# Optimization experiments

Measured on AMD Instinct MI355X. Metric: run time of the kernel, lower is better.

Reference implementation:

```python
import jax, jax.numpy as jnp
import numpy as np

H, HEADS, LAYERS = 512, 4, 3
HD = H // HEADS
FFN = 4 * H
B, S = 4, 2048
EPS = 1e-5
SCALE_BASE = 512.0
GAMMAS = (1.0 - np.exp(np.linspace(np.log(1.0 / 32.0), np.log(1.0 / 512.0), HEADS))).astype(np.float32)


def _xpos(x, downscale):
    # x: [B, heads, L, d]; standard XPOS rotary with per-dim decay scale
    L, d = x.shape[-2], x.shape[-1]
    half = d // 2
    s = (jnp.arange(half, dtype=jnp.float32) + 0.4 * d) / (1.4 * d)          # [half]
    pos = jnp.arange(L, dtype=jnp.float32)
    scale = s[None, :] ** (pos[:, None] / SCALE_BASE)                         # [L, half]
    inv_freq = 1.0 / (10000.0 ** (jnp.arange(half, dtype=jnp.float32) / half))
    ang = pos[:, None] * inv_freq[None, :]                                    # [L, half]
    if downscale:
        scale = 1.0 / scale
    sin_s = jnp.repeat(jnp.sin(ang) * scale, 2, axis=-1)                      # [L, d]
    cos_s = jnp.repeat(jnp.cos(ang) * scale, 2, axis=-1)
    x1, x2 = x[..., 0::2], x[..., 1::2]
    rot = jnp.stack([-x2, x1], axis=-1).reshape(x.shape)                      # rotate_every_two
    return x * cos_s + rot * sin_s


def _layernorm(x, w, b):
    m = x.mean(-1, keepdims=True)
    v = ((x - m) ** 2).mean(-1, keepdims=True)
    return (x - m) / jnp.sqrt(v + EPS) * w + b


def _decay_mask(L):
    n = jnp.arange(L)
    nm = n[:, None] - n[None, :]
    g = jnp.asarray(GAMMAS)                                                   # [heads]
    # D[h,n,m] = gamma_h^(n-m) for n>=m else 0
    return jnp.where((nm >= 0)[None], g[:, None, None] ** jnp.maximum(nm, 0)[None], 0.0)


def _msr(X, WQ, WK, WV, WG, WO, gnw, gnb, D):
    # X: [B,S,H]; WQ/WK/WV: [heads,H,HD]; D: [heads,S,S]
    Q = _xpos(jnp.einsum('bsh,nhd->bnsd', X, WQ), False)
    K = _xpos(jnp.einsum('bsh,nhd->bnsd', X, WK), True)
    V = jnp.einsum('bsh,nhd->bnsd', X, WV)
    A = jnp.einsum('bnsd,bntd->bnst', Q, K) * D[None]                          # decay-weighted retention
    Y = jnp.einsum('bnst,bntd->bnsd', A, V)                                    # [B,heads,S,HD]
    Y = jnp.transpose(Y, (0, 2, 1, 3))                                         # [B,S,heads,HD] (head-major concat)
    m = Y.mean(-1, keepdims=True)
    v = ((Y - m) ** 2).mean(-1, keepdims=True)
    Yn = ((Y - m) / jnp.sqrt(v + EPS)).reshape(X.shape[0], X.shape[1], H) * gnw + gnb  # GroupNorm(heads, H)
    G = X @ WG
    return (G * jax.nn.sigmoid(G) * Yn) @ WO                                   # swish gate + out proj


def setup_inputs() -> dict:
    key = jax.random.key(0)
    ks = jax.random.split(key, 10)
    rn = lambda k, shape, sc: jax.random.normal(k, shape, jnp.float32) * sc
    return {
        'X': rn(ks[0], (B, S, H), 1.0),
        'WQ': rn(ks[1], (LAYERS, HEADS, H, HD), 1.0 / H),
        'WK': rn(ks[2], (LAYERS, HEADS, H, HD), 1.0 / H),
        'WV': rn(ks[3], (LAYERS, HEADS, H, HD), 1.0 / H),
        'WG': rn(ks[4], (LAYERS, H, H), 1.0 / H),
        'WO': rn(ks[5], (LAYERS, H, H), 1.0 / H),
        'gn_w': jnp.ones((LAYERS, H), jnp.float32),
        'gn_b': jnp.zeros((LAYERS, H), jnp.float32),
        'ln1_w': jnp.ones((LAYERS, H), jnp.float32),
        'ln1_b': jnp.zeros((LAYERS, H), jnp.float32),
        'ln2_w': jnp.ones((LAYERS, H), jnp.float32),
        'ln2_b': jnp.zeros((LAYERS, H), jnp.float32),
        'ffn_w1': rn(ks[6], (LAYERS, H, FFN), (2.0 / (H + FFN)) ** 0.5),
        'ffn_b1': jnp.zeros((LAYERS, FFN), jnp.float32),
        'ffn_w2': rn(ks[7], (LAYERS, FFN, H), (2.0 / (H + FFN)) ** 0.5),
        'ffn_b2': jnp.zeros((LAYERS, H), jnp.float32),
    }


def reference(X, WQ, WK, WV, WG, WO, gn_w, gn_b, ln1_w, ln1_b, ln2_w, ln2_b, ffn_w1, ffn_b1, ffn_w2, ffn_b2):
    D = _decay_mask(X.shape[1])
    for l in range(LAYERS):
        Y = _msr(_layernorm(X, ln1_w[l], ln1_b[l]), WQ[l], WK[l], WV[l], WG[l], WO[l], gn_w[l], gn_b[l], D) + X
        Hn = _layernorm(Y, ln2_w[l], ln2_b[l])
        X = jax.nn.gelu(Hn @ ffn_w1[l] + ffn_b1[l], approximate=False) @ ffn_w2[l] + ffn_b2[l] + Y
    return X, jnp.einsum('bsh,bth->bst', X, X)
```

## Files before the change

### kernel.cpp

```cpp
#include <hip/hip_runtime.h>
#include <math.h>

#define HH 512
#define NHEADS 4
#define HD 128
#define HALF 64
#define FFND 2048
#define BB 4
#define SS 2048
#define NLAYERS 3
#define ROWS (BB*SS)
#define EPSF 1e-5f
#define QKVGW 2048

typedef float f32x4 __attribute__((ext_vector_type(4)));
typedef float f32x16 __attribute__((ext_vector_type(16)));
typedef __bf16 bf16x8 __attribute__((ext_vector_type(8)));
typedef unsigned u32x2 __attribute__((ext_vector_type(2)));

__device__ __forceinline__ unsigned short f2bf(float f) {
    union { float f; unsigned u; } v; v.f = f;
    unsigned r = (v.u + 0x7FFFu + ((v.u >> 16) & 1u)) >> 16;
    return (unsigned short)r;
}
__device__ __forceinline__ float bf2f(unsigned short h) {
    union { unsigned u; float f; } v; v.u = ((unsigned)h) << 16;
    return v.f;
}
__device__ __forceinline__ void gl16(const void* g, void* l) {
    __builtin_amdgcn_global_load_lds((const __attribute__((address_space(1))) void*)g,
                                     (__attribute__((address_space(3))) void*)l, 16, 0, 0);
}
__device__ __forceinline__ bf16x8 ld8(const void* p) { return *(const bf16x8*)p; }
__device__ __forceinline__ unsigned laddr(void* p) {
    return (unsigned)(size_t)(__attribute__((address_space(3))) char*)p;
}
__device__ __forceinline__ u32x2 tr8(unsigned a) {
    u32x2 r;
    asm volatile("ds_read_b64_tr_b16 %0, %1" : "=v"(r) : "v"(a));
    return r;
}

__global__ void k_tables(float* __restrict__ cq, float* __restrict__ sq,
                         float* __restrict__ ck, float* __restrict__ sk) {
    int i = threadIdx.x;
    int s = blockIdx.x;
    float si   = ((float)i + 0.4f * (float)HD) / (1.4f * (float)HD);
    float scale = powf(si, (float)s / 512.0f);
    float invf = powf(10000.0f, -((float)i) / (float)HALF);
    float ang  = (float)s * invf;
    float c = cosf(ang), sn = sinf(ang);
    int idx = s * HALF + i;
    cq[idx] = c * scale;   sq[idx] = sn * scale;
    float is = 1.0f / scale;
    ck[idx] = c * is;      sk[idx] = sn * is;
}

__global__ __launch_bounds__(256) void k_wt(const float* __restrict__ src, unsigned short* __restrict__ dst,
                                            int K, int N, int zn, size_t sL, size_t sZ) {
    __shared__ float T[32][33];
    int n0 = blockIdx.x * 32, k0 = blockIdx.y * 32;
    int z = blockIdx.z;
    src += (size_t)z * (size_t)K * N;
    dst += (size_t)(z / zn) * sL + (size_t)(z % zn) * sZ;
    int tx = threadIdx.x & 31, ty = threadIdx.x >> 5;
    #pragma unroll
    for (int i = 0; i < 4; ++i) {
        int r = ty + i * 8;
        T[r][tx] = src[(size_t)(k0 + r) * N + n0 + tx];
    }
    __syncthreads();
    #pragma unroll
    for (int i = 0; i < 4; ++i) {
        int r = ty + i * 8;
        dst[(size_t)(n0 + r) * K + k0 + tx] = f2bf(T[tx][r]);
    }
}

__global__ __launch_bounds__(256) void k_ln(const float* __restrict__ x, const float* __restrict__ w,
                                            const float* __restrict__ b, unsigned short* __restrict__ y) {
    int lane = threadIdx.x & 63;
    size_t row = (size_t)blockIdx.x * 4 + (threadIdx.x >> 6);
    const float4* xr = (const float4*)(x + row * HH);
    float4 v0 = xr[lane * 2];
    float4 v1 = xr[lane * 2 + 1];
    float s  = v0.x + v0.y + v0.z + v0.w + v1.x + v1.y + v1.z + v1.w;
    float ss = v0.x*v0.x + v0.y*v0.y + v0.z*v0.z + v0.w*v0.w
             + v1.x*v1.x + v1.y*v1.y + v1.z*v1.z + v1.w*v1.w;
    for (int off = 32; off > 0; off >>= 1) {
        s  += __shfl_xor(s, off);
        ss += __shfl_xor(ss, off);
    }
    float m   = s * (1.0f / HH);
    float var = ss * (1.0f / HH) - m * m;
    float inv = rsqrtf(var + EPSF);
    int h0 = lane * 8;
    float4 wa = *(const float4*)(w + h0);
    float4 wb = *(const float4*)(w + h0 + 4);
    float4 ba = *(const float4*)(b + h0);
    float4 bb2 = *(const float4*)(b + h0 + 4);
    uint4 pk;
    pk.x = f2bf((v0.x - m) * inv * wa.x + ba.x) | ((unsigned)f2bf((v0.y - m) * inv * wa.y + ba.y) << 16);
    pk.y = f2bf((v0.z - m) * inv * wa.z + ba.z) | ((unsigned)f2bf((v0.w - m) * inv * wa.w + ba.w) << 16);
    pk.z = f2bf((v1.x - m) * inv * wb.x + bb2.x) | ((unsigned)f2bf((v1.y - m) * inv * wb.y + bb2.y) << 16);
    pk.w = f2bf((v1.z - m) * inv * wb.z + bb2.z) | ((unsigned)f2bf((v1.w - m) * inv * wb.w + bb2.w) << 16);
    *(uint4*)(y + row * HH + h0) = pk;
}

__global__ __launch_bounds__(256) void k_xpos(unsigned short* __restrict__ QG,
    const float* __restrict__ cq, const float* __restrict__ sq,
    const float* __restrict__ ck, const float* __restrict__ sk) {
    int row = blockIdx.x, p = threadIdx.x;
    int s = row & (SS - 1), n = p >> 6, i = p & 63;
    int ti = s * HALF + i;
    size_t qo = (size_t)row * QKVGW + n * HD + i * 2;
    unsigned qv = *(unsigned*)(QG + qo);
    float x1 = bf2f(qv & 0xffff), x2 = bf2f(qv >> 16);
    float c = cq[ti], sn = sq[ti];
    *(unsigned*)(QG + qo) = (unsigned)f2bf(x1 * c - x2 * sn) | ((unsigned)f2bf(x2 * c + x1 * sn) << 16);
    size_t ko = qo + 512;
    unsigned kv = *(unsigned*)(QG + ko);
    x1 = bf2f(kv & 0xffff); x2 = bf2f(kv >> 16);
    c = ck[ti]; sn = sk[ti];
    *(unsigned*)(QG + ko) = (unsigned)f2bf(x1 * c - x2 * sn) | ((unsigned)f2bf(x2 * c + x1 * sn) << 16);
}

__global__ __launch_bounds__(128, 2) void k_ret(
    const unsigned short* __restrict__ QG, float* __restrict__ Y) {
    __shared__ __align__(16) char sm[40960];
    const int tid = threadIdx.x;
    const int lane = tid & 63, wv = tid >> 6;
    const int l31 = lane & 31, g2 = lane >> 5;
    const int b4 = (lane >> 4) & 1;
    const int xs = (int)gridDim.x - 1 - (int)blockIdx.x;
    const int hn = blockIdx.y, b = blockIdx.z;
    const int s0 = xs * 64;
    const double la = -3.4657359027997265, lb = -6.238324625039508;
    const float gamma = (float)(1.0 - exp(la + (lb - la) * ((double)hn / 3.0)));
    const float l2g = log2f(gamma);
    const size_t rowbase = (size_t)b * SS;
    const int qcol = hn * HD, kcol = 512 + hn * HD, vcol = 1024 + hn * HD;
    const char* Gp = (const char*)QG;

    const int srow = s0 + wv * 32 + l31;
    bf16x8 qf[8];
    #pragma unroll
    for (int kc = 0; kc < 8; ++kc)
        qf[kc] = ld8(QG + (rowbase + srow) * QKVGW + qcol + kc * 16 + g2 * 8);

    float gq[4], gj[4];
    #pragma unroll
    for (int q = 0; q < 4; ++q) { gq[q] = exp2f(-l2g * (8.0f * q)); gj[q] = exp2f(-l2g * (float)q); }
    const float gt32m = exp2f(-l2g * 32.0f);

    f32x16 accy[4];
    #pragma unroll
    for (int d = 0; d < 4; ++d)
        #pragma unroll
        for (int e = 0; e < 16; ++e) accy[d][e] = 0.0f;

    const int sloc = wv * 32 + l31;
    const int ssw = (sloc & 7) << 4;
    const int r15 = (l31 & 15) << 4;
    const unsigned vbase = laddr(sm + 16384) + b4 * 2048 + g2 * 256 + (lane & 15) * 2;
    const int nt = xs + 1;

    for (int t = 0; t < nt; ++t) {
        const int t0 = t * 64;
        __syncthreads();
        #pragma unroll
        for (int c = 0; c < 8; ++c) {
            int chunk = wv * 8 + c;
            int r = chunk * 4 + (lane >> 4);
            int w = ((lane & 15) * 16) ^ ((r & 15) << 4);
            gl16(Gp + ((rowbase + t0 + r) * QKVGW + kcol) * 2 + w, sm + chunk * 1024);
        }
        #pragma unroll
        for (int c = 0; c < 8; ++c) {
            int chunk = wv * 8 + c;
            int slot = chunk * 64 + lane;
            int sub = slot >> 3, w8 = slot & 7;
            int db = sub >> 4, tb = sub & 15;
            int tl = tb * 4 + (w8 >> 1);
            int d  = db * 16 + (w8 & 1) * 8;
            gl16(Gp + ((rowbase + t0 + tl) * QKVGW + vcol + d) * 2, sm + 16384 + chunk * 1024);
        }
        __syncthreads();
        f32x16 pacc0, pacc1;
        #pragma unroll
        for (int e = 0; e < 16; ++e) { pacc0[e] = 0.0f; pacc1[e] = 0.0f; }
        #pragma unroll
        for (int kc = 0; kc < 8; ++kc) {
            bf16x8 k0 = ld8(sm + l31 * 256 + ((kc * 32 + g2 * 16) ^ r15));
            bf16x8 k1 = ld8(sm + (32 + l31) * 256 + ((kc * 32 + g2 * 16) ^ r15));
            pacc0 = __builtin_amdgcn_mfma_f32_32x32x16_bf16(k0, qf[kc], pacc0, 0, 0, 0);
            pacc1 = __builtin_amdgcn_mfma_f32_32x32x16_bf16(k1, qf[kc], pacc1, 0, 0, 0);
        }
        const float G0 = exp2f(l2g * (float)(srow - t0 - g2 * 4));
        #pragma unroll
        for (int tb2 = 0; tb2 < 2; ++tb2) {
            const float gb = tb2 ? gt32m : 1.0f;
            #pragma unroll
            for (int q = 0; q < 4; ++q) {
                unsigned short u0, u1, u2, u3;
                int tbase = t0 + tb2 * 32 + q * 8 + g2 * 4;
                float base = G0 * gb * gq[q];
                float p0 = (tb2 ? pacc1 : pacc0)[q * 4 + 0];
                float p1 = (tb2 ? pacc1 : pacc0)[q * 4 + 1];
                float p2 = (tb2 ? pacc1 : pacc0)[q * 4 + 2];
                float p3 = (tb2 ? pacc1 : pacc0)[q * 4 + 3];
                u0 = f2bf((srow >= tbase + 0) ? p0 * base * gj[0] : 0.0f);
                u1 = f2bf((srow >= tbase + 1) ? p1 * base * gj[1] : 0.0f);
                u2 = f2bf((srow >= tbase + 2) ? p2 * base * gj[2] : 0.0f);
                u3 = f2bf((srow >= tbase + 3) ? p3 * base * gj[3] : 0.0f);
                u32x2 pk2;
                pk2.x = (unsigned)u0 | ((unsigned)u1 << 16);
                pk2.y = (unsigned)u2 | ((unsigned)u3 << 16);
                *(u32x2*)(sm + 32768 + ((sloc * 128 + tb2 * 64 + q * 16 + g2 * 8) ^ ssw)) = pk2;
            }
        }
        bf16x8 pf[4];
        #pragma unroll
        for (int tc = 0; tc < 4; ++tc)
            pf[tc] = ld8(sm + 32768 + ((sloc * 128 + tc * 32 + g2 * 16) ^ ssw));
        #pragma unroll
        for (int dblk = 0; dblk < 4; ++dblk) {
            u32x2 va[4], vb[4];
            #pragma unroll
            for (int tc = 0; tc < 4; ++tc) {
                unsigned a0 = vbase + dblk * 4096 + tc * 512;
                va[tc] = tr8(a0);
                vb[tc] = tr8(a0 + 128);
            }
            asm volatile("s_waitcnt lgkmcnt(0)" ::: "memory");
            __builtin_amdgcn_sched_barrier(0);
            #pragma unroll
            for (int tc = 0; tc < 4; ++tc) {
                union { u32x2 u[2]; bf16x8 v; } cvt;
                cvt.u[0] = va[tc]; cvt.u[1] = vb[tc];
                accy[dblk] = __builtin_amdgcn_mfma_f32_32x32x16_bf16(pf[tc], cvt.v, accy[dblk], 0, 0, 0);
            }
        }
    }
    #pragma unroll
    for (int dblk = 0; dblk < 4; ++dblk)
        #pragma unroll
        for (int rg = 0; rg < 16; ++rg) {
            int sl2 = s0 + wv * 32 + (rg & 3) + (rg >> 2) * 8 + g2 * 4;
            Y[(rowbase + sl2) * HH + hn * HD + dblk * 32 + l31] = accy[dblk][rg];
        }
}

__global__ __launch_bounds__(256) void k_gate(
    const float* __restrict__ Yr, const unsigned short* __restrict__ QG,
    const float* __restrict__ gw, const float* __restrict__ gb,
    unsigned short* __restrict__ E) {
    int lane = threadIdx.x & 63;
    int grp  = blockIdx.x * 4 + (threadIdx.x >> 6);
    int row = grp >> 2, nh = grp & 3;
    size_t off = (size_t)row * HH + nh * HD + lane * 2;
    float2 v = *(const float2*)(Yr + off);
    float s = v.x + v.y, ss = v.x * v.x + v.y * v.y;
    for (int o = 32; o > 0; o >>= 1) {
        s  += __shfl_xor(s, o);
        ss += __shfl_xor(ss, o);
    }
    float m   = s * (1.0f / HD);
    float var = ss * (1.0f / HD) - m * m;
    float inv = rsqrtf(var + EPSF);
    int h = nh * HD + lane * 2;
    unsigned gv = *(const unsigned*)(QG + (size_t)row * QKVGW + 1536 + nh * HD + lane * 2);
    float g0 = bf2f(gv & 0xffff), g1 = bf2f(gv >> 16);
    float2 w2 = *(const float2*)(gw + h), b2 = *(const float2*)(gb + h);
    float yn0 = (v.x - m) * inv * w2.x + b2.x;
    float yn1 = (v.y - m) * inv * w2.y + b2.y;
    float e0v = g0 / (1.0f + expf(-g0)) * yn0;
    float e1v = g1 / (1.0f + expf(-g1)) * yn1;
    *(unsigned*)(E + off) = (unsigned)f2bf(e0v) | ((unsigned)f2bf(e1v) << 16);
}

__global__ __launch_bounds__(256) void k_cast(const float* __restrict__ x, unsigned short* __restrict__ y) {
    size_t i = ((size_t)blockIdx.x * 256 + threadIdx.x) * 8;
    float4 a = *(const float4*)(x + i), c = *(const float4*)(x + i + 4);
    uint4 pk;
    pk.x = f2bf(a.x) | ((unsigned)f2bf(a.y) << 16);
    pk.y = f2bf(a.z) | ((unsigned)f2bf(a.w) << 16);
    pk.z = f2bf(c.x) | ((unsigned)f2bf(c.y) << 16);
    pk.w = f2bf(c.z) | ((unsigned)f2bf(c.w) << 16);
    *(uint4*)(y + i) = pk;
}

template<int EPI, int OUTBF>
__global__ __launch_bounds__(256) void k_mm(
    const unsigned short* __restrict__ A, const unsigned short* __restrict__ Bt,
    void* __restrict__ Cv, const float* __restrict__ bias, const float* __restrict__ Rs,
    int M, int N, int K, size_t aB, size_t bB, size_t cB) {
    __shared__ __align__(16) char sm[16384];
    const int tid = threadIdx.x;
    const int lane = tid & 63, wid = tid >> 6;
    const int wr = wid >> 1, wc = wid & 1;
    const int lcol = lane & 15, lrow = lane >> 4;
    const size_t m0 = (size_t)blockIdx.x * 128, n0 = (size_t)blockIdx.y * 128;
    const char* Ab = (const char*)(A + (size_t)blockIdx.z * aB);
    const char* Bb = (const char*)(Bt + (size_t)blockIdx.z * bB);
    f32x4 acc[4][4];
    #pragma unroll
    for (int i = 0; i < 4; ++i)
        #pragma unroll
        for (int j = 0; j < 4; ++j) acc[i][j] = f32x4{0.f, 0.f, 0.f, 0.f};
    for (int k0 = 0; k0 < K; k0 += 32) {
        __syncthreads();
        #pragma unroll
        for (int c = 0; c < 2; ++c) {
            int chunk = wid * 2 + c;
            int r = chunk * 16 + (lane >> 2);
            int w = ((lane & 3) ^ (r & 3)) << 4;
            gl16(Ab + ((size_t)(m0 + r) * K + k0) * 2 + w, sm + chunk * 1024);
            gl16(Bb + ((size_t)(n0 + r) * K + k0) * 2 + w, sm + 8192 + chunk * 1024);
        }
        __syncthreads();
        bf16x8 af[4], bfr[4];
        #pragma unroll
        for (int m = 0; m < 4; ++m) {
            int r = wr * 64 + m * 16 + lcol;
            af[m] = ld8(sm + r * 64 + ((lrow * 16) ^ ((r & 3) << 4)));
        }
        #pragma unroll
        for (int n2 = 0; n2 < 4; ++n2) {
            int r = wc * 64 + n2 * 16 + lcol;
            bfr[n2] = ld8(sm + 8192 + r * 64 + ((lrow * 16) ^ ((r & 3) << 4)));
        }
        #pragma unroll
        for (int m = 0; m < 4; ++m)
            #pragma unroll
            for (int n2 = 0; n2 < 4; ++n2)
                acc[m][n2] = __builtin_amdgcn_mfma_f32_16x16x32_bf16(af[m], bfr[n2], acc[m][n2], 0, 0, 0);
    }
    float* Cf = (float*)Cv + (size_t)blockIdx.z * cB;
    unsigned short* Cb = (unsigned short*)Cv + (size_t)blockIdx.z * cB;
    const float* Rb = (EPI >= 2) ? (Rs + (size_t)blockIdx.z * cB) : nullptr;
    #pragma unroll
    for (int m = 0; m < 4; ++m) {
        #pragma unroll
        for (int n2 = 0; n2 < 4; ++n2) {
            size_t col = n0 + wc * 64 + n2 * 16 + lcol;
            float bc = (EPI == 1 || EPI == 2) ? bias[col] : 0.0f;
            #pragma unroll
            for (int j = 0; j < 4; ++j) {
                size_t row = m0 + wr * 64 + m * 16 + lrow * 4 + j;
                float v = acc[m][n2][j];
                if (EPI == 1) { v += bc; v = 0.5f * v * (1.0f + erff(v * 0.70710678118654752f)); }
                else if (EPI == 2) v += bc + Rb[row * N + col];
                else if (EPI == 3) v += Rb[row * N + col];
                if (OUTBF) Cb[row * N + col] = f2bf(v);
                else       Cf[row * N + col] = v;
            }
        }
    }
}

extern "C" void kernel_launch(void* const* d_in, const int* in_sizes, int n_in,
                              void* d_out, int out_size, void* d_ws, size_t ws_size,
                              hipStream_t stream) {
    const float* X0  = (const float*)d_in[0];
    const float* WQ  = (const float*)d_in[1];
    const float* WK  = (const float*)d_in[2];
    const float* WV  = (const float*)d_in[3];
    const float* WG  = (const float*)d_in[4];
    const float* WO  = (const float*)d_in[5];
    const float* gnw = (const float*)d_in[6];
    const float* gnb = (const float*)d_in[7];
    const float* l1w = (const float*)d_in[8];
    const float* l1b = (const float*)d_in[9];
    const float* l2w = (const float*)d_in[10];
    const float* l2b = (const float*)d_in[11];
    const float* fw1 = (const float*)d_in[12];
    const float* fb1 = (const float*)d_in[13];
    const float* fw2 = (const float*)d_in[14];
    const float* fb2 = (const float*)d_in[15];
    float* outX = (float*)d_out;
    float* outG = outX + (size_t)ROWS * HH;

    char* wp = (char*)d_ws;
    auto take = [&](size_t bytes) { char* p = wp; wp += (bytes + 255) & ~(size_t)255; return p; };
    float* cq = (float*)take((size_t)SS * HALF * 4);
    float* sq = (float*)take((size_t)SS * HALF * 4);
    float* ck = (float*)take((size_t)SS * HALF * 4);
    float* sk = (float*)take((size_t)SS * HALF * 4);
    unsigned short* Wcat = (unsigned short*)take((size_t)NLAYERS * QKVGW * HH * 2);
    unsigned short* WOt = (unsigned short*)take((size_t)NLAYERS * HH * HH * 2);
    unsigned short* F1t = (unsigned short*)take((size_t)NLAYERS * HH * FFND * 2);
    unsigned short* F2t = (unsigned short*)take((size_t)NLAYERS * HH * FFND * 2);
    unsigned short* Xn  = (unsigned short*)take((size_t)ROWS * HH * 2);
    unsigned short* QKVG = (unsigned short*)take((size_t)ROWS * QKVGW * 2);
    unsigned short* Eb  = (unsigned short*)take((size_t)ROWS * HH * 2);
    float* Yr   = (float*)take((size_t)ROWS * HH * 4);
    float* Y2   = (float*)take((size_t)ROWS * HH * 4);
    float* Xbuf = (float*)take((size_t)ROWS * HH * 4);
    unsigned short* Hb = (unsigned short*)take((size_t)ROWS * FFND * 2);
    unsigned short* Xb = Xn;

    k_tables<<<SS, HALF, 0, stream>>>(cq, sq, ck, sk);
    k_wt<<<dim3(4, 16, 12), 256, 0, stream>>>(WQ, Wcat, HH, HD, 4, (size_t)QKVGW * HH, (size_t)HD * HH);
    k_wt<<<dim3(4, 16, 12), 256, 0, stream>>>(WK, Wcat + (size_t)512 * HH, HH, HD, 4, (size_t)QKVGW * HH, (size_t)HD * HH);
    k_wt<<<dim3(4, 16, 12), 256, 0, stream>>>(WV, Wcat + (size_t)1024 * HH, HH, HD, 4, (size_t)QKVGW * HH, (size_t)HD * HH);
    k_wt<<<dim3(16, 16, 3), 256, 0, stream>>>(WG, Wcat + (size_t)1536 * HH, HH, HH, 1, (size_t)QKVGW * HH, 0);
    k_wt<<<dim3(16, 16, 3), 256, 0, stream>>>(WO, WOt, HH, HH, 1, (size_t)HH * HH, 0);
    k_wt<<<dim3(64, 16, 3), 256, 0, stream>>>(fw1, F1t, HH, FFND, 1, (size_t)HH * FFND, 0);
    k_wt<<<dim3(16, 64, 3), 256, 0, stream>>>(fw2, F2t, FFND, HH, 1, (size_t)FFND * HH, 0);

    const float* curX = X0;
    for (int l = 0; l < NLAYERS; ++l) {
        const unsigned short* Bc = Wcat + (size_t)l * QKVGW * HH;
        const unsigned short* Bo = WOt + (size_t)l * HH * HH;
        const unsigned short* B1 = F1t + (size_t)l * HH * FFND;
        const unsigned short* B2 = F2t + (size_t)l * HH * FFND;
        k_ln<<<ROWS / 4, 256, 0, stream>>>(curX, l1w + l * HH, l1b + l * HH, Xn);
        dim3 gq(ROWS / 128, QKVGW / 128, 1);
        k_mm<0, 1><<<gq, 256, 0, stream>>>(Xn, Bc, QKVG, nullptr, nullptr, ROWS, QKVGW, HH, 0, 0, 0);
        k_xpos<<<ROWS, 256, 0, stream>>>(QKVG, cq, sq, ck, sk);
        k_ret<<<dim3(SS / 64, NHEADS, BB), 128, 0, stream>>>(QKVG, Yr);
        k_gate<<<ROWS, 256, 0, stream>>>(Yr, QKVG, gnw + l * HH, gnb + l * HH, Eb);
        dim3 g1(ROWS / 128, HH / 128, 1);
        k_mm<3, 0><<<g1, 256, 0, stream>>>(Eb, Bo, Y2, nullptr, curX, ROWS, HH, HH, 0, 0, 0);
        k_ln<<<ROWS / 4, 256, 0, stream>>>(Y2, l2w + l * HH, l2b + l * HH, Xn);
        dim3 g2(ROWS / 128, FFND / 128, 1);
        k_mm<1, 1><<<g2, 256, 0, stream>>>(Xn, B1, Hb, fb1 + (size_t)l * FFND, nullptr, ROWS, FFND, HH, 0, 0, 0);
        float* newX = (l == NLAYERS - 1) ? outX : Xbuf;
        k_mm<2, 0><<<g1, 256, 0, stream>>>(Hb, B2, newX, fb2 + (size_t)l * HH, Y2, ROWS, HH, FFND, 0, 0, 0);
        curX = newX;
    }
    k_cast<<<ROWS * HH / (256 * 8), 256, 0, stream>>>(outX, Xb);
    dim3 g3(SS / 128, SS / 128, BB);
    k_mm<0, 0><<<g3, 256, 0, stream>>>(Xb, Xb, outG, nullptr, nullptr, SS, SS, HH,
                                       (size_t)SS * HH, (size_t)SS * HH, (size_t)SS * SS);
}
```

Before: 930.2 us.

## Split long retention rows across blocks with atomics and fuse final bf16 cast

The causal retention kernel's work grows with row-tile index, so long rows are split into chunks of up to 8 key tiles handled by separate blocks. The grid grows from 32 to 80 blocks per head and batch, and partial results are accumulated into a zeroed Y buffer with float atomics. This balances load across CUs at the cost of an extra memset, atomic traffic and non-deterministic summation order. Separately, the last FFN GEMM epilogue writes both the fp32 output and a bf16 copy, removing the standalone cast kernel.

```diff
diff --git a/kernel.cpp b/kernel.cpp
--- a/kernel.cpp
+++ b/kernel.cpp
@@ -132,9 +132,16 @@
     const int lane = tid & 63, wv = tid >> 6;
     const int l31 = lane & 31, g2 = lane >> 5;
     const int b4 = (lane >> 4) & 1;
-    const int xs = (int)gridDim.x - 1 - (int)blockIdx.x;
+    const int bx = blockIdx.x;
+    int xs, c0;
+    if (bx < 32)      { xs = 24 + (bx >> 2); c0 = bx & 3; }
+    else if (bx < 56) { int i = bx - 32; int d = i / 3; xs = 16 + d; c0 = i - d * 3; }
+    else if (bx < 72) { int i = bx - 56; xs = 8 + (i >> 1); c0 = i & 1; }
+    else              { xs = bx - 72; c0 = 0; }
     const int hn = blockIdx.y, b = blockIdx.z;
     const int s0 = xs * 64;
+    const int tstart = c0 * 8;
+    const int tend = min(xs + 1, tstart + 8);
     const double la = -3.4657359027997265, lb = -6.238324625039508;
     const float gamma = (float)(1.0 - exp(la + (lb - la) * ((double)hn / 3.0)));
     const float l2g = log2f(gamma);
@@ -163,9 +170,8 @@
     const int ssw = (sloc & 7) << 4;
     const int r15 = (l31 & 15) << 4;
     const unsigned vbase = laddr(sm + 16384) + b4 * 2048 + g2 * 256 + (lane & 15) * 2;
-    const int nt = xs + 1;
-
-    for (int t = 0; t < nt; ++t) {
+
+    for (int t = tstart; t < tend; ++t) {
         const int t0 = t * 64;
         __syncthreads();
         #pragma unroll
@@ -242,13 +248,23 @@
             }
         }
     }
-    #pragma unroll
-    for (int dblk = 0; dblk < 4; ++dblk)
-        #pragma unroll
-        for (int rg = 0; rg < 16; ++rg) {
-            int sl2 = s0 + wv * 32 + (rg & 3) + (rg >> 2) * 8 + g2 * 4;
-            Y[(rowbase + sl2) * HH + hn * HD + dblk * 32 + l31] = accy[dblk][rg];
-        }
+    if (xs < 8) {
+        #pragma unroll
+        for (int dblk = 0; dblk < 4; ++dblk)
+            #pragma unroll
+            for (int rg = 0; rg < 16; ++rg) {
+                int sl2 = s0 + wv * 32 + (rg & 3) + (rg >> 2) * 8 + g2 * 4;
+                Y[(rowbase + sl2) * HH + hn * HD + dblk * 32 + l31] = accy[dblk][rg];
+            }
+    } else {
+        #pragma unroll
+        for (int dblk = 0; dblk < 4; ++dblk)
+            #pragma unroll
+            for (int rg = 0; rg < 16; ++rg) {
+                int sl2 = s0 + wv * 32 + (rg & 3) + (rg >> 2) * 8 + g2 * 4;
+                unsafeAtomicAdd(&Y[(rowbase + sl2) * HH + hn * HD + dblk * 32 + l31], accy[dblk][rg]);
+            }
+    }
 }
 
 __global__ __launch_bounds__(256) void k_gate(
@@ -279,22 +295,12 @@
     *(unsigned*)(E + off) = (unsigned)f2bf(e0v) | ((unsigned)f2bf(e1v) << 16);
 }
 
-__global__ __launch_bounds__(256) void k_cast(const float* __restrict__ x, unsigned short* __restrict__ y) {
-    size_t i = ((size_t)blockIdx.x * 256 + threadIdx.x) * 8;
-    float4 a = *(const float4*)(x + i), c = *(const float4*)(x + i + 4);
-    uint4 pk;
-    pk.x = f2bf(a.x) | ((unsigned)f2bf(a.y) << 16);
-    pk.y = f2bf(a.z) | ((unsigned)f2bf(a.w) << 16);
-    pk.z = f2bf(c.x) | ((unsigned)f2bf(c.y) << 16);
-    pk.w = f2bf(c.z) | ((unsigned)f2bf(c.w) << 16);
-    *(uint4*)(y + i) = pk;
-}
-
 template<int EPI, int OUTBF>
 __global__ __launch_bounds__(256) void k_mm(
     const unsigned short* __restrict__ A, const unsigned short* __restrict__ Bt,
     void* __restrict__ Cv, const float* __restrict__ bias, const float* __restrict__ Rs,
-    int M, int N, int K, size_t aB, size_t bB, size_t cB) {
+    int M, int N, int K, size_t aB, size_t bB, size_t cB,
+    unsigned short* __restrict__ C2) {
     __shared__ __align__(16) char sm[16384];
     const int tid = threadIdx.x;
     const int lane = tid & 63, wid = tid >> 6;
@@ -344,16 +350,19 @@
         #pragma unroll
         for (int n2 = 0; n2 < 4; ++n2) {
             size_t col = n0 + wc * 64 + n2 * 16 + lcol;
-            float bc = (EPI == 1 || EPI == 2) ? bias[col] : 0.0f;
+            float bc = (EPI == 1 || EPI == 2 || EPI == 4) ? bias[col] : 0.0f;
             #pragma unroll
             for (int j = 0; j < 4; ++j) {
                 size_t row = m0 + wr * 64 + m * 16 + lrow * 4 + j;
                 float v = acc[m][n2][j];
                 if (EPI == 1) { v += bc; v = 0.5f * v * (1.0f + erff(v * 0.70710678118654752f)); }
-                else if (EPI == 2) v += bc + Rb[row * N + col];
+                else if (EPI == 2 || EPI == 4) v += bc + Rb[row * N + col];
                 else if (EPI == 3) v += Rb[row * N + col];
-                if (OUTBF) Cb[row * N + col] = f2bf(v);
-                else       Cf[row * N + col] = v;
+                if (EPI == 4) {
+                    Cf[row * N + col] = v;
+                    C2[row * N + col] = f2bf(v);
+                } else if (OUTBF) Cb[row * N + col] = f2bf(v);
+                else              Cf[row * N + col] = v;
             }
         }
     }
@@ -417,21 +426,24 @@
         const unsigned short* B2 = F2t + (size_t)l * HH * FFND;
         k_ln<<<ROWS / 4, 256, 0, stream>>>(curX, l1w + l * HH, l1b + l * HH, Xn);
         dim3 gq(ROWS / 128, QKVGW / 128, 1);
-        k_mm<0, 1><<<gq, 256, 0, stream>>>(Xn, Bc, QKVG, nullptr, nullptr, ROWS, QKVGW, HH, 0, 0, 0);
+        k_mm<0, 1><<<gq, 256, 0, stream>>>(Xn, Bc, QKVG, nullptr, nullptr, ROWS, QKVGW, HH, 0, 0, 0, nullptr);
         k_xpos<<<ROWS, 256, 0, stream>>>(QKVG, cq, sq, ck, sk);
-        k_ret<<<dim3(SS / 64, NHEADS, BB), 128, 0, stream>>>(QKVG, Yr);
+        hipMemsetAsync(Yr, 0, (size_t)ROWS * HH * 4, stream);
+        k_ret<<<dim3(80, NHEADS, BB), 128, 0, stream>>>(QKVG, Yr);
         k_gate<<<ROWS, 256, 0, stream>>>(Yr, QKVG, gnw + l * HH, gnb + l * HH, Eb);
         dim3 g1(ROWS / 128, HH / 128, 1);
-        k_mm<3, 0><<<g1, 256, 0, stream>>>(Eb, Bo, Y2, nullptr, curX, ROWS, HH, HH, 0, 0, 0);
+        k_mm<3, 0><<<g1, 256, 0, stream>>>(Eb, Bo, Y2, nullptr, curX, ROWS, HH, HH, 0, 0, 0, nullptr);
         k_ln<<<ROWS / 4, 256, 0, stream>>>(Y2, l2w + l * HH, l2b + l * HH, Xn);
         dim3 g2(ROWS / 128, FFND / 128, 1);
-        k_mm<1, 1><<<g2, 256, 0, stream>>>(Xn, B1, Hb, fb1 + (size_t)l * FFND, nullptr, ROWS, FFND, HH, 0, 0, 0);
-        float* newX = (l == NLAYERS - 1) ? outX : Xbuf;
-        k_mm<2, 0><<<g1, 256, 0, stream>>>(Hb, B2, newX, fb2 + (size_t)l * HH, Y2, ROWS, HH, FFND, 0, 0, 0);
-        curX = newX;
-    }
-    k_cast<<<ROWS * HH / (256 * 8), 256, 0, stream>>>(outX, Xb);
+        k_mm<1, 1><<<g2, 256, 0, stream>>>(Xn, B1, Hb, fb1 + (size_t)l * FFND, nullptr, ROWS, FFND, HH, 0, 0, 0, nullptr);
+        if (l == NLAYERS - 1) {
+            k_mm<4, 0><<<g1, 256, 0, stream>>>(Hb, B2, outX, fb2 + (size_t)l * HH, Y2, ROWS, HH, FFND, 0, 0, 0, Xb);
+        } else {
+            k_mm<2, 0><<<g1, 256, 0, stream>>>(Hb, B2, Xbuf, fb2 + (size_t)l * HH, Y2, ROWS, HH, FFND, 0, 0, 0, nullptr);
+        }
+        curX = Xbuf;
+    }
     dim3 g3(SS / 128, SS / 128, BB);
     k_mm<0, 0><<<g3, 256, 0, stream>>>(Xb, Xb, outG, nullptr, nullptr, SS, SS, HH,
-                                       (size_t)SS * HH, (size_t)SS * HH, (size_t)SS * SS);
-}
+                                       (size_t)SS * HH, (size_t)SS * HH, (size_t)SS * SS, nullptr);
+}
```

Measured after the change: 893.1 us. 1.04x faster.
